# Optimization experiments

Hardware: AMD Instinct MI355X
Metric: run time of the kernel (lower is better)

The kernel has to match this reference:

```python
import jax, jax.numpy as jnp
import numpy as np


def _layernorm(x, g, b, eps=1e-5):
    mu = jnp.mean(x, axis=-1, keepdims=True)
    var = jnp.mean(jnp.square(x - mu), axis=-1, keepdims=True)
    return (x - mu) * jax.lax.rsqrt(var + eps) * g + b


def setup_inputs() -> dict:
    key = jax.random.key(0)
    ks = jax.random.split(key, 8)
    B, S, E, K, H = 32, 64, 768, 36, 4
    w = 0.02
    return {
        "x": jax.random.normal(ks[0], (B, S, E), dtype=jnp.float32),
        "y": jax.random.normal(ks[1], (B * S, K, E), dtype=jnp.float32),
        "ln_gamma": jnp.ones((H, E), jnp.float32),
        "ln_beta": jnp.zeros((H, E), jnp.float32),
        "W1": jax.random.normal(ks[2], (H, E, E), dtype=jnp.float32) * w,
        "b1": jnp.zeros((H, E), jnp.float32),
        "W2x": jax.random.normal(ks[3], (H, E), dtype=jnp.float32) * w,  # first half of Linear(2E,1)
        "W2y": jax.random.normal(ks[4], (H, E), dtype=jnp.float32) * w,  # second half of Linear(2E,1)
        "b2": jnp.zeros((H,), jnp.float32),
        "Wm": jax.random.normal(ks[5], (H * E, E), dtype=jnp.float32) * w,
        "bm": jnp.zeros((E,), jnp.float32),
        "select_indegree_num": 36,
    }


def reference(x, y, ln_gamma, ln_beta, W1, b1, W2x, W2y, b2, Wm, bm, select_indegree_num):
    # x: [B,S,E], y: [B*S,K,E]; dropout layers are identity in eval mode.
    B, S, E = x.shape
    H = ln_gamma.shape[0]
    xf = x.reshape(B * S, E)
    outs = []
    for h in range(H):
        # shared linear1 (LayerNorm + Linear) applied to both x and y
        x_ = _layernorm(xf, ln_gamma[h], ln_beta[h]) @ W1[h] + b1[h]          # [BS,E]
        y_ = _layernorm(y, ln_gamma[h], ln_beta[h]) @ W1[h] + b1[h]           # [BS,K,E]
        logit = (x_ @ W2x[h])[:, None] + y_ @ W2y[h] + b2[h]                  # [BS,K]
        prob = jax.nn.softmax(logit, axis=1)                                   # softmax over neighbors
        a = jnp.einsum('nk,nke->ne', prob, y_)                                 # weighted sum, [BS,E]
        outs.append(jax.nn.gelu(xf + a))                                       # GELU(x + a)
    cat = jnp.concatenate(outs, axis=-1)                                       # [BS,H*E]
    res = jax.nn.gelu(cat @ Wm + bm).reshape(B, S, E)
    return x + res  # has_residual=True
```

## Files before the change

### kernel.cpp

```cpp
#include <hip/hip_runtime.h>
#include <hip/hip_bf16.h>
#include <math.h>

#define EE 768
#define HH 4
#define KK 36
#define BSN 2048

typedef __attribute__((ext_vector_type(8))) short short8;
typedef __attribute__((ext_vector_type(4))) short short4v;
typedef __attribute__((ext_vector_type(4))) float float4v;

__device__ inline short f2bf(float x){
  return __builtin_bit_cast(short, __float2bfloat16(x));
}
__device__ inline float bf2f(short s){
  return __bfloat162float(__builtin_bit_cast(__hip_bfloat16, s));
}
__device__ inline float gelu_tanh(float x){
  float t = tanhf(0.79788456080286536f * (x + 0.044715f * x * x * x));
  return 0.5f * x * (1.0f + t);
}

__global__ __launch_bounds__(256) void k_v(const float* __restrict__ W1,
                                           const float* __restrict__ W2y,
                                           const float* __restrict__ g,
                                           const float* __restrict__ b1,
                                           float* __restrict__ v,
                                           float* __restrict__ b1p){
  const int wid  = blockIdx.x * 4 + (threadIdx.x >> 6);
  const int lane = threadIdx.x & 63;
  const int h = wid / EE, e = wid % EE;
  const float* W  = W1 + ((size_t)h * EE + e) * EE;
  const float* wy = W2y + h * EE;
  float acc = 0.f;
  #pragma unroll
  for (int j = 0; j < 12; ++j){
    int f = lane + 64 * j;
    acc += W[f] * wy[f];
  }
  #pragma unroll
  for (int off = 32; off; off >>= 1) acc += __shfl_xor(acc, off);
  if (lane == 0) v[h * EE + e] = g[h * EE + e] * acc;

  int idx = blockIdx.x * 256 + threadIdx.x;
  if (idx < HH * EE) b1p[idx] = b1[idx];
}

__global__ __launch_bounds__(256) void k_b1p_acc(const float* __restrict__ W1,
                                                 const float* __restrict__ beta,
                                                 float* __restrict__ b1p){
  const int h   = blockIdx.x >> 6;
  const int ec0 = (blockIdx.x & 63) * 12;
  const float* W  = W1 + (size_t)h * EE * EE;
  const float* bt = beta + h * EE;
  const int f = threadIdx.x;
  float a0 = 0.f, a1 = 0.f, a2 = 0.f;
  #pragma unroll
  for (int e = ec0; e < ec0 + 12; ++e){
    float be = bt[e];
    const float* row = W + (size_t)e * EE;
    a0 += be * row[f];
    a1 += be * row[f + 256];
    a2 += be * row[f + 512];
  }
  atomicAdd(&b1p[h * EE + f],       a0);
  atomicAdd(&b1p[h * EE + f + 256], a1);
  atomicAdd(&b1p[h * EE + f + 512], a2);
}

__global__ __launch_bounds__(256) void k_tW1(const float* __restrict__ W1,
                                             const float* __restrict__ g,
                                             short* __restrict__ W1t){
  __shared__ float tile[32][33];
  const int h  = blockIdx.z;
  const int e0 = blockIdx.x * 32, f0 = blockIdx.y * 32;
  const int tx = threadIdx.x & 31, ty = threadIdx.x >> 5;
  const float* W = W1 + (size_t)h * EE * EE;
  #pragma unroll
  for (int i = 0; i < 4; ++i){
    int e = e0 + ty + 8 * i;
    tile[ty + 8 * i][tx] = W[(size_t)e * EE + f0 + tx] * g[h * EE + e];
  }
  __syncthreads();
  #pragma unroll
  for (int i = 0; i < 4; ++i){
    int f = f0 + ty + 8 * i;
    W1t[((size_t)h * EE + f) * EE + e0 + tx] = f2bf(tile[tx][ty + 8 * i]);
  }
}

__global__ __launch_bounds__(256) void k_tWm(const float* __restrict__ Wm,
                                             short* __restrict__ Wmt){
  __shared__ float tile[32][33];
  const int c0 = blockIdx.x * 32, f0 = blockIdx.y * 32;
  const int tx = threadIdx.x & 31, ty = threadIdx.x >> 5;
  #pragma unroll
  for (int i = 0; i < 4; ++i){
    tile[ty + 8 * i][tx] = Wm[(size_t)(c0 + ty + 8 * i) * EE + f0 + tx];
  }
  __syncthreads();
  #pragma unroll
  for (int i = 0; i < 4; ++i){
    Wmt[(size_t)(f0 + ty + 8 * i) * (HH * EE) + c0 + tx] = f2bf(tile[tx][ty + 8 * i]);
  }
}

__global__ __launch_bounds__(256) void k_pass_y(const float* __restrict__ y,
                                                const float* __restrict__ v,
                                                short* __restrict__ p_y){
  const int wave = threadIdx.x >> 6, lane = threadIdx.x & 63;
  const int n = blockIdx.x * 4 + wave;
  const float* base = y + (size_t)n * KK * EE + 4 * lane;

  float4v vreg[HH][3];
  #pragma unroll
  for (int h = 0; h < HH; ++h)
    #pragma unroll
    for (int j = 0; j < 3; ++j)
      vreg[h][j] = *(const float4v*)(v + h * EE + 4 * lane + 256 * j);

  float4v acc[HH][3];
  #pragma unroll
  for (int h = 0; h < HH; ++h)
    #pragma unroll
    for (int j = 0; j < 3; ++j)
      acc[h][j] = (float4v){0.f, 0.f, 0.f, 0.f};
  float m[HH], l[HH];
  #pragma unroll
  for (int h = 0; h < HH; ++h){ m[h] = -INFINITY; l[h] = 0.f; }

  float4v bufA[3], bufB[3];
  #pragma unroll
  for (int j = 0; j < 3; ++j) bufA[j] = *(const float4v*)(base + 256 * j);
  #pragma unroll
  for (int j = 0; j < 3; ++j) bufB[j] = *(const float4v*)(base + EE + 256 * j);

  #pragma unroll 2
  for (int k = 0; k < KK; ++k){
    float4v cur[3];
    #pragma unroll
    for (int j = 0; j < 3; ++j) cur[j] = bufA[j];
    #pragma unroll
    for (int j = 0; j < 3; ++j) bufA[j] = bufB[j];
    if (k + 2 < KK){
      const float* rp = base + (size_t)(k + 2) * EE;
      #pragma unroll
      for (int j = 0; j < 3; ++j) bufB[j] = *(const float4v*)(rp + 256 * j);
    }

    float s = 0.f, s2 = 0.f;
    #pragma unroll
    for (int j = 0; j < 3; ++j)
      #pragma unroll
      for (int c = 0; c < 4; ++c){ float t = cur[j][c]; s += t; s2 += t * t; }
    #pragma unroll
    for (int off = 32; off; off >>= 1){
      s  += __shfl_xor(s, off);
      s2 += __shfl_xor(s2, off);
    }
    const float mu = s * (1.f / EE);
    const float rs = rsqrtf(s2 * (1.f / EE) - mu * mu + 1e-5f);

    float d[HH] = {0.f, 0.f, 0.f, 0.f};
    #pragma unroll
    for (int j = 0; j < 3; ++j)
      #pragma unroll
      for (int c = 0; c < 4; ++c){
        float t = (cur[j][c] - mu) * rs;
        cur[j][c] = t;
        d[0] += t * vreg[0][j][c];
        d[1] += t * vreg[1][j][c];
        d[2] += t * vreg[2][j][c];
        d[3] += t * vreg[3][j][c];
      }
    #pragma unroll
    for (int off = 32; off; off >>= 1){
      d[0] += __shfl_xor(d[0], off);
      d[1] += __shfl_xor(d[1], off);
      d[2] += __shfl_xor(d[2], off);
      d[3] += __shfl_xor(d[3], off);
    }

    #pragma unroll
    for (int h = 0; h < HH; ++h){
      if (d[h] > m[h]){
        float sc = __expf(m[h] - d[h]);
        l[h] *= sc;
        #pragma unroll
        for (int j = 0; j < 3; ++j)
          #pragma unroll
          for (int c = 0; c < 4; ++c) acc[h][j][c] *= sc;
        m[h] = d[h];
      }
      float w = __expf(d[h] - m[h]);
      l[h] += w;
      #pragma unroll
      for (int j = 0; j < 3; ++j)
        #pragma unroll
        for (int c = 0; c < 4; ++c) acc[h][j][c] += w * cur[j][c];
    }
  }

  #pragma unroll
  for (int h = 0; h < HH; ++h){
    const float inv = 1.f / l[h];
    #pragma unroll
    for (int j = 0; j < 3; ++j){
      short4v pk;
      #pragma unroll
      for (int c = 0; c < 4; ++c) pk[c] = f2bf(acc[h][j][c] * inv);
      *(short4v*)(p_y + ((size_t)h * BSN + n) * EE + 4 * lane + 256 * j) = pk;
    }
  }
}

template<int MODE>
__global__ __launch_bounds__(256) void k_gemm(const short* __restrict__ A,
                                              const short* __restrict__ Bt,
                                              const float* __restrict__ addv,
                                              const float* __restrict__ x,
                                              void* __restrict__ out,
                                              int Kdim, size_t strideA, size_t strideB){
  __shared__ short As[64][72];
  __shared__ short Bs[64][72];
  const int z = blockIdx.z;
  const short* Ah = A + strideA * z;
  const short* Bh = Bt + strideB * z;
  const float* addh = addv + (size_t)768 * z;

  const int tid = threadIdx.x;
  const int wave = tid >> 6, lane = tid & 63;
  const int quad = lane >> 4, l16 = lane & 15;
  const int m0 = blockIdx.x * 64, n0 = blockIdx.y * 64;
  const int r = tid >> 3, c8 = (tid & 7) * 8;

  float4v acc[4];
  #pragma unroll
  for (int t = 0; t < 4; ++t) acc[t] = (float4v){0.f, 0.f, 0.f, 0.f};

  const short* Ap0 = Ah + (size_t)(m0 + r) * Kdim + c8;
  const short* Ap1 = Ah + (size_t)(m0 + r + 32) * Kdim + c8;
  const short* Bp0 = Bh + (size_t)(n0 + r) * Kdim + c8;
  const short* Bp1 = Bh + (size_t)(n0 + r + 32) * Kdim + c8;

  for (int k0 = 0; k0 < Kdim; k0 += 64){
    short8 a0 = *(const short8*)(Ap0 + k0);
    short8 a1 = *(const short8*)(Ap1 + k0);
    short8 b0 = *(const short8*)(Bp0 + k0);
    short8 b1 = *(const short8*)(Bp1 + k0);
    __syncthreads();
    *(short8*)(&As[r][c8])      = a0;
    *(short8*)(&As[r + 32][c8]) = a1;
    *(short8*)(&Bs[r][c8])      = b0;
    *(short8*)(&Bs[r + 32][c8]) = b1;
    __syncthreads();
    #pragma unroll
    for (int kk = 0; kk < 64; kk += 32){
      short8 bf = *(const short8*)(&Bs[16 * wave + l16][kk + quad * 8]);
      #pragma unroll
      for (int t = 0; t < 4; ++t){
        short8 af = *(const short8*)(&As[16 * t + l16][kk + quad * 8]);
        acc[t] = __builtin_amdgcn_mfma_f32_16x16x32_bf16(af, bf, acc[t], 0, 0, 0);
      }
    }
  }

  const int f = n0 + 16 * wave + l16;
  const float add = addh[f];
  #pragma unroll
  for (int t = 0; t < 4; ++t){
    #pragma unroll
    for (int rr = 0; rr < 4; ++rr){
      const int m = m0 + 16 * t + quad * 4 + rr;
      const float val = acc[t][rr] + add;
      const float xf = x[(size_t)m * EE + f];
      if (MODE == 0){
        ((short*)out)[(size_t)m * (HH * EE) + 768 * z + f] = f2bf(gelu_tanh(xf + val));
      } else {
        ((float*)out)[(size_t)m * EE + f] = xf + gelu_tanh(val);
      }
    }
  }
}

extern "C" void kernel_launch(void* const* d_in, const int* in_sizes, int n_in,
                              void* d_out, int out_size, void* d_ws, size_t ws_size,
                              hipStream_t stream){
  const float* x    = (const float*)d_in[0];
  const float* y    = (const float*)d_in[1];
  const float* g    = (const float*)d_in[2];
  const float* beta = (const float*)d_in[3];
  const float* W1   = (const float*)d_in[4];
  const float* b1   = (const float*)d_in[5];
  const float* W2y  = (const float*)d_in[7];
  const float* Wm   = (const float*)d_in[9];
  const float* bm   = (const float*)d_in[10];

  char* ws = (char*)d_ws;
  float* v    = (float*)(ws + 0);
  float* b1p  = (float*)(ws + 12288);
  short* W1t  = (short*)(ws + 24576);
  short* Wmt  = (short*)(ws + 4743168);
  short* p_y  = (short*)(ws + 9461760);
  short* catb = (short*)(ws + 22044672);
  float* out  = (float*)d_out;

  k_v<<<dim3(768), dim3(256), 0, stream>>>(W1, W2y, g, b1, v, b1p);
  k_b1p_acc<<<dim3(256), dim3(256), 0, stream>>>(W1, beta, b1p);
  k_tW1<<<dim3(24, 24, 4), dim3(256), 0, stream>>>(W1, g, W1t);
  k_tWm<<<dim3(96, 24), dim3(256), 0, stream>>>(Wm, Wmt);
  k_pass_y<<<dim3(512), dim3(256), 0, stream>>>(y, v, p_y);
  k_gemm<0><<<dim3(32, 12, 4), dim3(256), 0, stream>>>(
      p_y, W1t, b1p, x, (void*)catb, 768, (size_t)2048 * 768, (size_t)768 * 768);
  k_gemm<1><<<dim3(32, 12, 1), dim3(256), 0, stream>>>(
      catb, Wmt, bm, x, (void*)out, 3072, (size_t)0, (size_t)0);
}
```

Measured before the change: 444.0 us.

## Use 128x128 MFMA GEMM tiles with direct global-to-LDS loads and split-K

Both GEMMs move from 64x64 tiles with one MFMA column per wave to 128x128 tiles where each wave computes a 64x64 sub-tile. Operands are loaded straight into LDS with global_load_lds, skipping the register staging step. The final GEMM is split along K into two halves that write fp32 partial sums, and a new elementwise kernel adds them with bias, GELU and the residual. The goal is more data reuse per LDS load and enough blocks in flight for the final GEMM. In exchange it adds a partial-sum buffer round trip, drops the LDS padding (possible bank conflicts), and uses single-buffered loads with no overlap.

```diff
diff --git a/kernel.cpp b/kernel.cpp
--- a/kernel.cpp
+++ b/kernel.cpp
@@ -20,6 +20,12 @@
 __device__ inline float gelu_tanh(float x){
   float t = tanhf(0.79788456080286536f * (x + 0.044715f * x * x * x));
   return 0.5f * x * (1.0f + t);
+}
+__device__ __forceinline__ void gload_lds16(const short* g, short* l){
+  __builtin_amdgcn_global_load_lds(
+      (const __attribute__((address_space(1))) void*)g,
+      (__attribute__((address_space(3))) void*)l,
+      16, 0, 0);
 }
 
 __global__ __launch_bounds__(256) void k_v(const float* __restrict__ W1,
@@ -216,72 +222,109 @@
 }
 
 template<int MODE>
-__global__ __launch_bounds__(256) void k_gemm(const short* __restrict__ A,
-                                              const short* __restrict__ Bt,
-                                              const float* __restrict__ addv,
-                                              const float* __restrict__ x,
-                                              void* __restrict__ out,
-                                              int Kdim, size_t strideA, size_t strideB){
-  __shared__ short As[64][72];
-  __shared__ short Bs[64][72];
+__global__ __launch_bounds__(256) void k_gemm128(const short* __restrict__ A,
+                                                 const short* __restrict__ Bt,
+                                                 const float* __restrict__ addv,
+                                                 const float* __restrict__ x,
+                                                 void* __restrict__ out,
+                                                 int Kdim, size_t strideA, size_t strideB){
+  __shared__ short As[128 * 64];
+  __shared__ short Bs[128 * 64];
   const int z = blockIdx.z;
-  const short* Ah = A + strideA * z;
-  const short* Bh = Bt + strideB * z;
-  const float* addh = addv + (size_t)768 * z;
+  const short* Ah; const short* Bh; int kbeg, kend;
+  if (MODE == 0){ Ah = A + strideA * z; Bh = Bt + strideB * z; kbeg = 0; kend = Kdim; }
+  else          { Ah = A; Bh = Bt; kbeg = z * (Kdim >> 1); kend = kbeg + (Kdim >> 1); }
 
   const int tid = threadIdx.x;
-  const int wave = tid >> 6, lane = tid & 63;
+  const int w = tid >> 6, lane = tid & 63;
   const int quad = lane >> 4, l16 = lane & 15;
-  const int m0 = blockIdx.x * 64, n0 = blockIdx.y * 64;
-  const int r = tid >> 3, c8 = (tid & 7) * 8;
-
-  float4v acc[4];
-  #pragma unroll
-  for (int t = 0; t < 4; ++t) acc[t] = (float4v){0.f, 0.f, 0.f, 0.f};
-
-  const short* Ap0 = Ah + (size_t)(m0 + r) * Kdim + c8;
-  const short* Ap1 = Ah + (size_t)(m0 + r + 32) * Kdim + c8;
-  const short* Bp0 = Bh + (size_t)(n0 + r) * Kdim + c8;
-  const short* Bp1 = Bh + (size_t)(n0 + r + 32) * Kdim + c8;
-
-  for (int k0 = 0; k0 < Kdim; k0 += 64){
-    short8 a0 = *(const short8*)(Ap0 + k0);
-    short8 a1 = *(const short8*)(Ap1 + k0);
-    short8 b0 = *(const short8*)(Bp0 + k0);
-    short8 b1 = *(const short8*)(Bp1 + k0);
+  const int m0 = blockIdx.x * 128, n0 = blockIdx.y * 128;
+  const int lr = lane >> 3;
+  const int lc = (lane & 7) * 8;
+
+  const short* gA = Ah + (size_t)(m0 + w * 32 + lr) * Kdim + lc;
+  const short* gB = Bh + (size_t)(n0 + w * 32 + lr) * Kdim + lc;
+  short* lA = As + (w * 32) * 64;
+  short* lB = Bs + (w * 32) * 64;
+
+  float4v acc[4][4];
+  #pragma unroll
+  for (int mt = 0; mt < 4; ++mt)
+    #pragma unroll
+    for (int nt = 0; nt < 4; ++nt) acc[mt][nt] = (float4v){0.f, 0.f, 0.f, 0.f};
+
+  const int wm = (w & 1) * 64, wn = (w >> 1) * 64;
+
+  for (int k0 = kbeg; k0 < kend; k0 += 64){
     __syncthreads();
-    *(short8*)(&As[r][c8])      = a0;
-    *(short8*)(&As[r + 32][c8]) = a1;
-    *(short8*)(&Bs[r][c8])      = b0;
-    *(short8*)(&Bs[r + 32][c8]) = b1;
+    #pragma unroll
+    for (int i = 0; i < 4; ++i){
+      gload_lds16(gA + (size_t)(8 * i) * Kdim + k0, lA + i * 8 * 64);
+      gload_lds16(gB + (size_t)(8 * i) * Kdim + k0, lB + i * 8 * 64);
+    }
     __syncthreads();
     #pragma unroll
     for (int kk = 0; kk < 64; kk += 32){
-      short8 bf = *(const short8*)(&Bs[16 * wave + l16][kk + quad * 8]);
-      #pragma unroll
-      for (int t = 0; t < 4; ++t){
-        short8 af = *(const short8*)(&As[16 * t + l16][kk + quad * 8]);
-        acc[t] = __builtin_amdgcn_mfma_f32_16x16x32_bf16(af, bf, acc[t], 0, 0, 0);
-      }
-    }
-  }
-
-  const int f = n0 + 16 * wave + l16;
-  const float add = addh[f];
-  #pragma unroll
-  for (int t = 0; t < 4; ++t){
-    #pragma unroll
-    for (int rr = 0; rr < 4; ++rr){
-      const int m = m0 + 16 * t + quad * 4 + rr;
-      const float val = acc[t][rr] + add;
-      const float xf = x[(size_t)m * EE + f];
-      if (MODE == 0){
-        ((short*)out)[(size_t)m * (HH * EE) + 768 * z + f] = f2bf(gelu_tanh(xf + val));
-      } else {
-        ((float*)out)[(size_t)m * EE + f] = xf + gelu_tanh(val);
-      }
-    }
-  }
+      short8 afr[4], bfr[4];
+      #pragma unroll
+      for (int nt = 0; nt < 4; ++nt)
+        bfr[nt] = *(const short8*)(Bs + (wn + nt * 16 + l16) * 64 + kk + quad * 8);
+      #pragma unroll
+      for (int mt = 0; mt < 4; ++mt)
+        afr[mt] = *(const short8*)(As + (wm + mt * 16 + l16) * 64 + kk + quad * 8);
+      #pragma unroll
+      for (int mt = 0; mt < 4; ++mt)
+        #pragma unroll
+        for (int nt = 0; nt < 4; ++nt)
+          acc[mt][nt] = __builtin_amdgcn_mfma_f32_16x16x32_bf16(afr[mt], bfr[nt], acc[mt][nt], 0, 0, 0);
+    }
+  }
+
+  if (MODE == 0){
+    const float* addh = addv + 768 * z;
+    #pragma unroll
+    for (int nt = 0; nt < 4; ++nt){
+      const int f = n0 + wn + nt * 16 + l16;
+      const float add = addh[f];
+      #pragma unroll
+      for (int mt = 0; mt < 4; ++mt)
+        #pragma unroll
+        for (int rr = 0; rr < 4; ++rr){
+          const int m = m0 + wm + mt * 16 + quad * 4 + rr;
+          const float val = acc[mt][nt][rr] + add;
+          const float xf = x[(size_t)m * EE + f];
+          ((short*)out)[(size_t)m * (HH * EE) + 768 * z + f] = f2bf(gelu_tanh(xf + val));
+        }
+    }
+  } else {
+    float* po = (float*)out + (size_t)z * BSN * EE;
+    #pragma unroll
+    for (int nt = 0; nt < 4; ++nt){
+      const int f = n0 + wn + nt * 16 + l16;
+      #pragma unroll
+      for (int mt = 0; mt < 4; ++mt)
+        #pragma unroll
+        for (int rr = 0; rr < 4; ++rr){
+          const int m = m0 + wm + mt * 16 + quad * 4 + rr;
+          po[(size_t)m * EE + f] = acc[mt][nt][rr];
+        }
+    }
+  }
+}
+
+__global__ __launch_bounds__(256) void k_ep(const float* __restrict__ part,
+                                            const float* __restrict__ bm,
+                                            const float* __restrict__ x,
+                                            float* __restrict__ out){
+  const size_t i = ((size_t)blockIdx.x * 256 + threadIdx.x) * 4;
+  float4v p0 = *(const float4v*)(part + i);
+  float4v p1 = *(const float4v*)(part + (size_t)BSN * EE + i);
+  float4v xv = *(const float4v*)(x + i);
+  float4v bv = *(const float4v*)(bm + (int)(i % EE));
+  float4v o;
+  #pragma unroll
+  for (int c = 0; c < 4; ++c) o[c] = xv[c] + gelu_tanh(p0[c] + p1[c] + bv[c]);
+  *(float4v*)(out + i) = o;
 }
 
 extern "C" void kernel_launch(void* const* d_in, const int* in_sizes, int n_in,
@@ -304,6 +347,7 @@
   short* Wmt  = (short*)(ws + 4743168);
   short* p_y  = (short*)(ws + 9461760);
   short* catb = (short*)(ws + 22044672);
+  float* part = (float*)(ws + 34627584);
   float* out  = (float*)d_out;
 
   k_v<<<dim3(768), dim3(256), 0, stream>>>(W1, W2y, g, b1, v, b1p);
@@ -311,8 +355,9 @@
   k_tW1<<<dim3(24, 24, 4), dim3(256), 0, stream>>>(W1, g, W1t);
   k_tWm<<<dim3(96, 24), dim3(256), 0, stream>>>(Wm, Wmt);
   k_pass_y<<<dim3(512), dim3(256), 0, stream>>>(y, v, p_y);
-  k_gemm<0><<<dim3(32, 12, 4), dim3(256), 0, stream>>>(
+  k_gemm128<0><<<dim3(16, 6, 4), dim3(256), 0, stream>>>(
       p_y, W1t, b1p, x, (void*)catb, 768, (size_t)2048 * 768, (size_t)768 * 768);
-  k_gemm<1><<<dim3(32, 12, 1), dim3(256), 0, stream>>>(
-      catb, Wmt, bm, x, (void*)out, 3072, (size_t)0, (size_t)0);
-}
+  k_gemm128<1><<<dim3(16, 6, 2), dim3(256), 0, stream>>>(
+      catb, Wmt, nullptr, nullptr, (void*)part, 3072, (size_t)0, (size_t)0);
+  k_ep<<<dim3(1536), dim3(256), 0, stream>>>(part, bm, x, out);
+}
```

Result: slower. 454.9 us (+2.5%).
